# Kernel optimization log

Hardware: AMD Instinct MI355X
Metric: run time of the kernel (lower is better)

## Reference

```python
import jax, jax.numpy as jnp
import numpy as np

NUM_EXPERTS = 8
TOP_K = 2


def setup_inputs() -> dict:
    key = jax.random.key(0)
    k1, k2, k3, k4, k5 = jax.random.split(key, 5)
    B, S, H, F, E = 4, 2048, 1024, 4096, NUM_EXPERTS
    return {
        "hidden_states": jax.random.normal(k1, (B, S, H), dtype=jnp.float32),
        "gate_w": jax.random.normal(k2, (E, H), dtype=jnp.float32) * 0.02,
        "w1": jax.random.normal(k3, (E, F, H), dtype=jnp.float32) * 0.02,
        "w3": jax.random.normal(k4, (E, F, H), dtype=jnp.float32) * 0.02,
        "w2": jax.random.normal(k5, (E, H, F), dtype=jnp.float32) * 0.02,
    }


def reference(hidden_states, gate_w, w1, w3, w2):
    B, S, H = hidden_states.shape
    E = gate_w.shape[0]
    x = hidden_states.reshape(-1, H)  # [T, H]
    T = x.shape[0]

    # Router: logits -> fp32 softmax -> top-k -> renormalize (Mixtral)
    router_logits = x @ gate_w.T  # [T, E]
    probs = jax.nn.softmax(router_logits.astype(jnp.float32), axis=-1)
    top_w, top_idx = jax.lax.top_k(probs, TOP_K)  # [T, K]
    top_w = top_w / jnp.sum(top_w, axis=-1, keepdims=True)
    top_w = top_w.astype(x.dtype)

    # Combine weights per (token, expert); zero for unselected experts.
    comb = jnp.zeros((T, E), dtype=x.dtype).at[
        jnp.arange(T)[:, None], top_idx
    ].add(top_w)  # [T, E]

    out = jnp.zeros((T, H), dtype=x.dtype)
    for e in range(E):  # structural loop over distinct expert weights
        h = jax.nn.silu(x @ w1[e].T) * (x @ w3[e].T)  # [T, F]
        out = out + comb[:, e:e + 1] * (h @ w2[e].T)  # [T, H]

    return out.reshape(B, S, H), router_logits
```

## Files before the change

### kernel.cpp

```cpp
#include <hip/hip_runtime.h>
#include <hip/hip_bf16.h>
#include <stdint.h>

#define T_TOK 8192
#define H_DIM 1024
#define F_DIM 4096
#define NEXP  8
#define CAP        17408
#define CT128      136

typedef __attribute__((ext_vector_type(8))) short bf16x8;
typedef __attribute__((ext_vector_type(4))) float f32x4;

#define AS1 __attribute__((address_space(1)))
#define AS3 __attribute__((address_space(3)))

__device__ __forceinline__ void gload_lds16(const void* g, void* l) {
  __builtin_amdgcn_global_load_lds((const AS1 void*)g, (AS3 void*)l, 16, 0, 0);
}

__device__ __forceinline__ int tile_expert_of(const int* counts, int tm) {
  int row = tm * 128, off = 0, e = NEXP - 1;
#pragma unroll
  for (int k = 0; k < NEXP; ++k) {
    int nxt = off + ((counts[k] + 127) & ~127);
    if (row >= off && row < nxt) { e = k; break; }
    off = nxt;
  }
  return e;
}

struct TK { int i0, i1; float w0, w1; };

__global__ __launch_bounds__(256) void router_kernel(
    const float* __restrict__ x, const float* __restrict__ gw,
    float* __restrict__ logits, int* __restrict__ counts, TK* __restrict__ tk)
{
  const int lane = threadIdx.x & 63;
  const int t = blockIdx.x * 4 + (threadIdx.x >> 6);
  const float* xp = x + (size_t)t * H_DIM;
  float xr[16];
#pragma unroll
  for (int i = 0; i < 16; ++i) xr[i] = xp[lane + i * 64];
  float lg[NEXP];
#pragma unroll
  for (int e = 0; e < NEXP; ++e) {
    const float* gp = gw + e * H_DIM;
    float acc = 0.f;
#pragma unroll
    for (int i = 0; i < 16; ++i) acc += xr[i] * gp[lane + i * 64];
#pragma unroll
    for (int s = 32; s > 0; s >>= 1) acc += __shfl_xor(acc, s, 64);
    lg[e] = acc;
  }
  if (lane < NEXP) logits[(size_t)t * NEXP + lane] = lg[lane];
  if (lane == 0) {
    int i0 = 0; float m0 = lg[0];
#pragma unroll
    for (int e = 1; e < NEXP; ++e) if (lg[e] > m0) { m0 = lg[e]; i0 = e; }
    int i1 = -1; float m1 = -1e30f;
#pragma unroll
    for (int e = 0; e < NEXP; ++e) if (e != i0 && lg[e] > m1) { m1 = lg[e]; i1 = e; }
    float r = expf(m1 - m0);
    float w0 = 1.f / (1.f + r);
    float w1 = r / (1.f + r);
    TK v; v.i0 = i0; v.i1 = i1; v.w0 = w0; v.w1 = w1;
    tk[t] = v;
    atomicAdd(&counts[i0], 1);
    atomicAdd(&counts[i1], 1);
  }
}

__global__ __launch_bounds__(256) void scatter_kernel(
    const TK* __restrict__ tk, const int* __restrict__ counts,
    int* __restrict__ cursor, int* __restrict__ pair_tok,
    float* __restrict__ pair_w, int2* __restrict__ inv)
{
  int t = blockIdx.x * 256 + threadIdx.x;
  if (t >= T_TOK) return;
  int offs[NEXP];
  int o = 0;
#pragma unroll
  for (int e = 0; e < NEXP; ++e) { offs[e] = o; o += (counts[e] + 127) & ~127; }
  TK v = tk[t];
  int p0 = offs[v.i0] + atomicAdd(&cursor[v.i0], 1);
  pair_tok[p0] = t; pair_w[p0] = v.w0;
  int p1 = offs[v.i1] + atomicAdd(&cursor[v.i1], 1);
  pair_tok[p1] = t; pair_w[p1] = v.w1;
  inv[t] = make_int2(p0, p1);
}

union Pack8 { __hip_bfloat16 o[8]; uint4 u; };

__global__ __launch_bounds__(256) void gather_kernel(
    const float* __restrict__ x, const int* __restrict__ pair_tok,
    __hip_bfloat16* __restrict__ xg)
{
  int idx = blockIdx.x * 256 + threadIdx.x;
  int row = idx >> 7;
  int c8  = (idx & 127) << 3;
  int tok = pair_tok[row];
  const float4* src = reinterpret_cast<const float4*>(x + (size_t)tok * H_DIM + c8);
  float4 a = src[0], b = src[1];
  Pack8 pk;
  pk.o[0] = __float2bfloat16(a.x); pk.o[1] = __float2bfloat16(a.y);
  pk.o[2] = __float2bfloat16(a.z); pk.o[3] = __float2bfloat16(a.w);
  pk.o[4] = __float2bfloat16(b.x); pk.o[5] = __float2bfloat16(b.y);
  pk.o[6] = __float2bfloat16(b.z); pk.o[7] = __float2bfloat16(b.w);
  *reinterpret_cast<uint4*>(xg + (size_t)row * H_DIM + c8) = pk.u;
}

__global__ __launch_bounds__(256) void convert3_kernel(
    const float* __restrict__ w1, const float* __restrict__ w3,
    const float* __restrict__ w2, __hip_bfloat16* __restrict__ w1b,
    __hip_bfloat16* __restrict__ w3b, __hip_bfloat16* __restrict__ w2b)
{
  const long long nthr = 3ll * (1 << 22);
  for (long long idx = (long long)blockIdx.x * 256 + threadIdx.x; idx < nthr;
       idx += (long long)gridDim.x * 256) {
    int seg = (int)(idx >> 22);
    long long off = (idx & ((1 << 22) - 1)) * 8;
    const float* src = (seg == 0) ? w1 : (seg == 1) ? w3 : w2;
    __hip_bfloat16* dst = (seg == 0) ? w1b : (seg == 1) ? w3b : w2b;
    float4 a = *reinterpret_cast<const float4*>(src + off);
    float4 b = *reinterpret_cast<const float4*>(src + off + 4);
    Pack8 pk;
    pk.o[0] = __float2bfloat16(a.x); pk.o[1] = __float2bfloat16(a.y);
    pk.o[2] = __float2bfloat16(a.z); pk.o[3] = __float2bfloat16(a.w);
    pk.o[4] = __float2bfloat16(b.x); pk.o[5] = __float2bfloat16(b.y);
    pk.o[6] = __float2bfloat16(b.z); pk.o[7] = __float2bfloat16(b.w);
    *reinterpret_cast<uint4*>(dst + off) = pk.u;
  }
}


__global__ __launch_bounds__(256, 4) void gemm1_kernel(
    const __hip_bfloat16* __restrict__ xg,
    const __hip_bfloat16* __restrict__ w1b,
    const __hip_bfloat16* __restrict__ w3b,
    const int* __restrict__ counts,
    __hip_bfloat16* __restrict__ h)
{
  __shared__ __hip_bfloat16 smem[16384];
  __hip_bfloat16* sA  = smem;
  __hip_bfloat16* sB1 = smem + 8192;
  __hip_bfloat16* sB3 = smem + 12288;

  const int n_  = blockIdx.x;
  const int tm  = n_ >> 6;
  const int tf  = n_ & 63;
  const int e   = tile_expert_of(counts, tm);
  const int tid = threadIdx.x;

  const __hip_bfloat16* A  = xg  + (size_t)tm * 128 * H_DIM;
  const __hip_bfloat16* B1 = w1b + (size_t)e * F_DIM * H_DIM + (size_t)tf * 64 * H_DIM;
  const __hip_bfloat16* B3 = w3b + (size_t)e * F_DIM * H_DIM + (size_t)tf * 64 * H_DIM;

  const int rs  = tid >> 3;
  const int sl  = tid & 7;
  const int xsl = (sl ^ (rs & 7)) * 8;
  const int dst = rs * 64 + sl * 8;

  const int wv = tid >> 6, lane = tid & 63;
  const int wm = wv >> 1, wn = wv & 1;
  const int l16 = lane & 15, lk = lane >> 4;
  const int ps0 = ((0 + lk) ^ (l16 & 7)) * 8;
  const int ps1 = ((4 + lk) ^ (l16 & 7)) * 8;

  f32x4 acc1[4][2] = {};
  f32x4 acc3[4][2] = {};

  for (int kt = 0; kt < H_DIM / 64; ++kt) {
    __syncthreads();
    const int gk = kt * 64 + xsl;
#pragma unroll
    for (int c = 0; c < 4; ++c)
      gload_lds16(A + (size_t)(rs + 32 * c) * H_DIM + gk, &sA[c * 2048 + dst]);
#pragma unroll
    for (int c = 0; c < 2; ++c) {
      gload_lds16(B1 + (size_t)(rs + 32 * c) * H_DIM + gk, &sB1[c * 2048 + dst]);
      gload_lds16(B3 + (size_t)(rs + 32 * c) * H_DIM + gk, &sB3[c * 2048 + dst]);
    }
    __syncthreads();
#pragma unroll
    for (int ks = 0; ks < 2; ++ks) {
      const int ps = ks ? ps1 : ps0;
      bf16x8 a[4], b1[2], b3[2];
#pragma unroll
      for (int m = 0; m < 4; ++m)
        a[m] = *reinterpret_cast<const bf16x8*>(&sA[(wm * 64 + m * 16 + l16) * 64 + ps]);
#pragma unroll
      for (int nf = 0; nf < 2; ++nf) {
        b1[nf] = *reinterpret_cast<const bf16x8*>(&sB1[(wn * 32 + nf * 16 + l16) * 64 + ps]);
        b3[nf] = *reinterpret_cast<const bf16x8*>(&sB3[(wn * 32 + nf * 16 + l16) * 64 + ps]);
      }
#pragma unroll
      for (int m = 0; m < 4; ++m)
#pragma unroll
        for (int nf = 0; nf < 2; ++nf) {
          acc1[m][nf] = __builtin_amdgcn_mfma_f32_16x16x32_bf16(a[m], b1[nf], acc1[m][nf], 0, 0, 0);
          acc3[m][nf] = __builtin_amdgcn_mfma_f32_16x16x32_bf16(a[m], b3[nf], acc3[m][nf], 0, 0, 0);
        }
    }
  }

  __syncthreads();
#pragma unroll
  for (int m = 0; m < 4; ++m)
#pragma unroll
    for (int nf = 0; nf < 2; ++nf)
#pragma unroll
      for (int j = 0; j < 4; ++j) {
        int row = wm * 64 + m * 16 + lk * 4 + j;
        int col = wn * 32 + nf * 16 + l16;
        int phys = row * 64 + (((col >> 3) ^ (row & 7)) << 3) + (col & 7);
        float c1 = acc1[m][nf][j];
        float c3 = acc3[m][nf][j];
        float s  = c1 / (1.f + expf(-c1));
        smem[phys] = __float2bfloat16(s * c3);
      }
  __syncthreads();
  const uint4* s4 = reinterpret_cast<const uint4*>(smem);
  __hip_bfloat16* hp = h + (size_t)tm * 128 * F_DIM + (size_t)tf * 64;
#pragma unroll
  for (int i = 0; i < 4; ++i) {
    int c = i * 256 + tid;
    int row = c >> 3, sg = c & 7;
    *reinterpret_cast<uint4*>(hp + (size_t)row * F_DIM + sg * 8) =
        s4[row * 8 + (sg ^ (row & 7))];
  }
}

__global__ __launch_bounds__(256, 4) void gemm2_kernel(
    const __hip_bfloat16* __restrict__ h,
    const __hip_bfloat16* __restrict__ w2b,
    const int* __restrict__ counts,
    const float* __restrict__ pair_w,
    __hip_bfloat16* __restrict__ y)
{
  __shared__ __hip_bfloat16 smem[16384];
  __hip_bfloat16* sA = smem;
  __hip_bfloat16* sB = smem + 8192;

  const int n_  = blockIdx.x;
  const int r   = n_ & 7;
  const int q   = n_ >> 3;
  const int tm  = (q >> 4) * 8 + r;
  const int s_  = q & 15;
  const int tn  = s_ >> 1;
  const int kh  = s_ & 1;
  const int e   = tile_expert_of(counts, tm);
  const int tid = threadIdx.x;

  const __hip_bfloat16* A = h   + (size_t)tm * 128 * F_DIM + (size_t)kh * 2048;
  const __hip_bfloat16* B = w2b + (size_t)e * H_DIM * F_DIM + (size_t)tn * 128 * F_DIM
                                + (size_t)kh * 2048;

  const int rs  = tid >> 3;
  const int sl  = tid & 7;
  const int xsl = (sl ^ (rs & 7)) * 8;
  const int dst = rs * 64 + sl * 8;

  const int wv = tid >> 6, lane = tid & 63;
  const int wm = wv >> 1, wn = wv & 1;
  const int l16 = lane & 15, lk = lane >> 4;
  const int ps0 = ((0 + lk) ^ (l16 & 7)) * 8;
  const int ps1 = ((4 + lk) ^ (l16 & 7)) * 8;

  f32x4 acc[4][4] = {};

  for (int kt = 0; kt < 2048 / 64; ++kt) {
    __syncthreads();
    const int gk = kt * 64 + xsl;
#pragma unroll
    for (int c = 0; c < 4; ++c) {
      gload_lds16(A + (size_t)(rs + 32 * c) * F_DIM + gk, &sA[c * 2048 + dst]);
      gload_lds16(B + (size_t)(rs + 32 * c) * F_DIM + gk, &sB[c * 2048 + dst]);
    }
    __syncthreads();
#pragma unroll
    for (int ks = 0; ks < 2; ++ks) {
      const int ps = ks ? ps1 : ps0;
      bf16x8 a[4], b[4];
#pragma unroll
      for (int m = 0; m < 4; ++m)
        a[m] = *reinterpret_cast<const bf16x8*>(&sA[(wm * 64 + m * 16 + l16) * 64 + ps]);
#pragma unroll
      for (int nf = 0; nf < 4; ++nf)
        b[nf] = *reinterpret_cast<const bf16x8*>(&sB[(wn * 64 + nf * 16 + l16) * 64 + ps]);
#pragma unroll
      for (int m = 0; m < 4; ++m)
#pragma unroll
        for (int nf = 0; nf < 4; ++nf)
          acc[m][nf] = __builtin_amdgcn_mfma_f32_16x16x32_bf16(a[m], b[nf], acc[m][nf], 0, 0, 0);
    }
  }

  __syncthreads();
#pragma unroll
  for (int m = 0; m < 4; ++m)
#pragma unroll
    for (int j = 0; j < 4; ++j) {
      int row  = wm * 64 + m * 16 + lk * 4 + j;
      float w  = pair_w[tm * 128 + row];
#pragma unroll
      for (int nf = 0; nf < 4; ++nf) {
        int col  = wn * 64 + nf * 16 + l16;
        int phys = row * 128 + (((col >> 3) ^ (row & 7)) << 3) + (col & 7);
        smem[phys] = __float2bfloat16(w * acc[m][nf][j]);
      }
    }
  __syncthreads();
  const uint4* s4 = reinterpret_cast<const uint4*>(smem);
  __hip_bfloat16* yp = y + (size_t)kh * CAP * H_DIM
                         + (size_t)tm * 128 * H_DIM + (size_t)tn * 128;
#pragma unroll
  for (int i = 0; i < 8; ++i) {
    int c = i * 256 + tid;
    int row = c >> 4, sg = c & 15;
    *reinterpret_cast<uint4*>(yp + (size_t)row * H_DIM + sg * 8) =
        s4[row * 16 + ((sg & 8) | ((sg ^ row) & 7))];
  }
}

__global__ __launch_bounds__(256) void combine_kernel(
    const __hip_bfloat16* __restrict__ y, const int2* __restrict__ inv,
    float* __restrict__ out)
{
  int idx = blockIdx.x * 256 + threadIdx.x;
  int t  = idx >> 7;
  int c8 = (idx & 127) << 3;
  int2 p = inv[t];
  const __hip_bfloat16* y1 = y + (size_t)CAP * H_DIM;
  union { uint4 u; __hip_bfloat16 o[8]; } a, b, c, d;
  a.u = *reinterpret_cast<const uint4*>(y  + (size_t)p.x * H_DIM + c8);
  b.u = *reinterpret_cast<const uint4*>(y  + (size_t)p.y * H_DIM + c8);
  c.u = *reinterpret_cast<const uint4*>(y1 + (size_t)p.x * H_DIM + c8);
  d.u = *reinterpret_cast<const uint4*>(y1 + (size_t)p.y * H_DIM + c8);
  float* op = out + (size_t)t * H_DIM + c8;
#pragma unroll
  for (int i = 0; i < 8; ++i)
    op[i] = __bfloat162float(a.o[i]) + __bfloat162float(b.o[i]) +
            __bfloat162float(c.o[i]) + __bfloat162float(d.o[i]);
}

#define WS_COUNTS   0
#define WS_CURSOR   32
#define WS_TK       1024
#define WS_PAIRTOK  132096
#define WS_PAIRW    201728
#define WS_ZERO_BYTES 271360
#define WS_INV      271360
#define WS_XG       336896ll
#define WS_W1       (WS_XG + 35651584ll)
#define WS_W3       (WS_W1 + 67108864ll)
#define WS_W2       (WS_W3 + 67108864ll)
#define WS_H        (WS_W2 + 67108864ll)
#define WS_Y        WS_XG

extern "C" void kernel_launch(void* const* d_in, const int* in_sizes, int n_in,
                              void* d_out, int out_size, void* d_ws, size_t ws_size,
                              hipStream_t stream) {
  const float* x  = (const float*)d_in[0];
  const float* gw = (const float*)d_in[1];
  const float* w1 = (const float*)d_in[2];
  const float* w3 = (const float*)d_in[3];
  const float* w2 = (const float*)d_in[4];
  float* out    = (float*)d_out;
  float* logits = out + (size_t)T_TOK * H_DIM;

  char* ws = (char*)d_ws;
  int*   counts   = (int*)(ws + WS_COUNTS);
  int*   cursor   = (int*)(ws + WS_CURSOR);
  TK*    tk       = (TK*)(ws + WS_TK);
  int*   pair_tok = (int*)(ws + WS_PAIRTOK);
  float* pair_w   = (float*)(ws + WS_PAIRW);
  int2*  inv      = (int2*)(ws + WS_INV);
  __hip_bfloat16* xg  = (__hip_bfloat16*)(ws + WS_XG);
  __hip_bfloat16* w1b = (__hip_bfloat16*)(ws + WS_W1);
  __hip_bfloat16* w3b = (__hip_bfloat16*)(ws + WS_W3);
  __hip_bfloat16* w2b = (__hip_bfloat16*)(ws + WS_W2);
  __hip_bfloat16* hbuf = (__hip_bfloat16*)(ws + WS_H);
  __hip_bfloat16* ybuf = (__hip_bfloat16*)(ws + WS_Y);

  hipMemsetAsync(d_ws, 0, WS_ZERO_BYTES, stream);

  router_kernel<<<T_TOK / 4, 256, 0, stream>>>(x, gw, logits, counts, tk);
  scatter_kernel<<<T_TOK / 256, 256, 0, stream>>>(tk, counts, cursor,
                                                  pair_tok, pair_w, inv);
  gather_kernel<<<(CAP * 128) / 256, 256, 0, stream>>>(x, pair_tok, xg);

  convert3_kernel<<<8192, 256, 0, stream>>>(w1, w3, w2, w1b, w3b, w2b);

  gemm1_kernel<<<CT128 * (F_DIM / 64), 256, 0, stream>>>(
      xg, w1b, w3b, counts, hbuf);
  gemm2_kernel<<<CT128 * 16, 256, 0, stream>>>(
      hbuf, w2b, counts, pair_w, ybuf);
  combine_kernel<<<(T_TOK * H_DIM / 8) / 256, 256, 0, stream>>>(ybuf, inv, out);
}
```

Before: 866.4 us.

## Enlarge gemm1 tiles to 256x128 with double-buffered LDS pipeline

Pads expert segments to 256 rows and rewrites the gate/up GEMM to use 512-thread blocks computing 256x128 tiles. The K loop now double-buffers LDS and interleaves the global-to-LDS loads for the next step with the MFMA work of the current step, using split barriers and s_setprio. This aims to raise data reuse per block and hide load latency. In exchange it adds more padding rows, raises register and LDS pressure, and leaves fewer blocks in the grid.

```diff
diff --git a/kernel.cpp b/kernel.cpp
--- a/kernel.cpp
+++ b/kernel.cpp
@@ -6,8 +6,9 @@
 #define H_DIM 1024
 #define F_DIM 4096
 #define NEXP  8
-#define CAP        17408
-#define CT128      136
+#define CAP        18432
+#define CT256      72
+#define CT128      144
 
 typedef __attribute__((ext_vector_type(8))) short bf16x8;
 typedef __attribute__((ext_vector_type(4))) float f32x4;
@@ -19,11 +20,11 @@
   __builtin_amdgcn_global_load_lds((const AS1 void*)g, (AS3 void*)l, 16, 0, 0);
 }
 
-__device__ __forceinline__ int tile_expert_of(const int* counts, int tm) {
-  int row = tm * 128, off = 0, e = NEXP - 1;
+__device__ __forceinline__ int expert_of_row(const int* counts, int row) {
+  int off = 0, e = NEXP - 1;
 #pragma unroll
   for (int k = 0; k < NEXP; ++k) {
-    int nxt = off + ((counts[k] + 127) & ~127);
+    int nxt = off + ((counts[k] + 255) & ~255);
     if (row >= off && row < nxt) { e = k; break; }
     off = nxt;
   }
@@ -81,7 +82,7 @@
   int offs[NEXP];
   int o = 0;
 #pragma unroll
-  for (int e = 0; e < NEXP; ++e) { offs[e] = o; o += (counts[e] + 127) & ~127; }
+  for (int e = 0; e < NEXP; ++e) { offs[e] = o; o += (counts[e] + 255) & ~255; }
   TK v = tk[t];
   int p0 = offs[v.i0] + atomicAdd(&cursor[v.i0], 1);
   pair_tok[p0] = t; pair_w[p0] = v.w0;
@@ -134,27 +135,25 @@
 }
 
 
-__global__ __launch_bounds__(256, 4) void gemm1_kernel(
+__global__ __launch_bounds__(512, 2) void gemm1_kernel(
     const __hip_bfloat16* __restrict__ xg,
     const __hip_bfloat16* __restrict__ w1b,
     const __hip_bfloat16* __restrict__ w3b,
     const int* __restrict__ counts,
     __hip_bfloat16* __restrict__ h)
 {
-  __shared__ __hip_bfloat16 smem[16384];
-  __hip_bfloat16* sA  = smem;
-  __hip_bfloat16* sB1 = smem + 8192;
-  __hip_bfloat16* sB3 = smem + 12288;
-
-  const int n_  = blockIdx.x;
-  const int tm  = n_ >> 6;
-  const int tf  = n_ & 63;
-  const int e   = tile_expert_of(counts, tm);
+  __shared__ __hip_bfloat16 sA[2][256 * 64];
+  __shared__ __hip_bfloat16 sB[2][256 * 64];
+
+  const int n_ = blockIdx.x;
+  const int tm = n_ >> 5;
+  const int tf = n_ & 31;
+  const int e  = expert_of_row(counts, tm * 256);
   const int tid = threadIdx.x;
 
-  const __hip_bfloat16* A  = xg  + (size_t)tm * 128 * H_DIM;
-  const __hip_bfloat16* B1 = w1b + (size_t)e * F_DIM * H_DIM + (size_t)tf * 64 * H_DIM;
-  const __hip_bfloat16* B3 = w3b + (size_t)e * F_DIM * H_DIM + (size_t)tf * 64 * H_DIM;
+  const __hip_bfloat16* A  = xg  + (size_t)tm * 256 * H_DIM;
+  const __hip_bfloat16* B1 = w1b + (size_t)e * F_DIM * H_DIM + (size_t)tf * 128 * H_DIM;
+  const __hip_bfloat16* B3 = w3b + (size_t)e * F_DIM * H_DIM + (size_t)tf * 128 * H_DIM;
 
   const int rs  = tid >> 3;
   const int sl  = tid & 7;
@@ -162,73 +161,102 @@
   const int dst = rs * 64 + sl * 8;
 
   const int wv = tid >> 6, lane = tid & 63;
-  const int wm = wv >> 1, wn = wv & 1;
+  const int wm = wv >> 2, wn = wv & 3;
   const int l16 = lane & 15, lk = lane >> 4;
   const int ps0 = ((0 + lk) ^ (l16 & 7)) * 8;
   const int ps1 = ((4 + lk) ^ (l16 & 7)) * 8;
 
-  f32x4 acc1[4][2] = {};
-  f32x4 acc3[4][2] = {};
-
-  for (int kt = 0; kt < H_DIM / 64; ++kt) {
-    __syncthreads();
-    const int gk = kt * 64 + xsl;
-#pragma unroll
-    for (int c = 0; c < 4; ++c)
-      gload_lds16(A + (size_t)(rs + 32 * c) * H_DIM + gk, &sA[c * 2048 + dst]);
-#pragma unroll
-    for (int c = 0; c < 2; ++c) {
-      gload_lds16(B1 + (size_t)(rs + 32 * c) * H_DIM + gk, &sB1[c * 2048 + dst]);
-      gload_lds16(B3 + (size_t)(rs + 32 * c) * H_DIM + gk, &sB3[c * 2048 + dst]);
-    }
-    __syncthreads();
-#pragma unroll
-    for (int ks = 0; ks < 2; ++ks) {
-      const int ps = ks ? ps1 : ps0;
-      bf16x8 a[4], b1[2], b3[2];
-#pragma unroll
-      for (int m = 0; m < 4; ++m)
-        a[m] = *reinterpret_cast<const bf16x8*>(&sA[(wm * 64 + m * 16 + l16) * 64 + ps]);
-#pragma unroll
-      for (int nf = 0; nf < 2; ++nf) {
-        b1[nf] = *reinterpret_cast<const bf16x8*>(&sB1[(wn * 32 + nf * 16 + l16) * 64 + ps]);
-        b3[nf] = *reinterpret_cast<const bf16x8*>(&sB3[(wn * 32 + nf * 16 + l16) * 64 + ps]);
+  f32x4 acc1[8][2] = {};
+  f32x4 acc3[8][2] = {};
+  bf16x8 a[4][2], b[2][2];
+
+#define ST_A01(bb, gg) { \
+    gload_lds16(A + (size_t)rs * H_DIM + (gg) + xsl,          &sA[bb][dst]); \
+    gload_lds16(A + (size_t)(64 + rs) * H_DIM + (gg) + xsl,   &sA[bb][4096 + dst]); }
+#define ST_A23(bb, gg) { \
+    gload_lds16(A + (size_t)(128 + rs) * H_DIM + (gg) + xsl,  &sA[bb][8192 + dst]); \
+    gload_lds16(A + (size_t)(192 + rs) * H_DIM + (gg) + xsl,  &sA[bb][12288 + dst]); }
+#define ST_B1(bb, gg) { \
+    gload_lds16(B1 + (size_t)rs * H_DIM + (gg) + xsl,         &sB[bb][dst]); \
+    gload_lds16(B1 + (size_t)(64 + rs) * H_DIM + (gg) + xsl,  &sB[bb][4096 + dst]); }
+#define ST_B3(bb, gg) { \
+    gload_lds16(B3 + (size_t)rs * H_DIM + (gg) + xsl,         &sB[bb][8192 + dst]); \
+    gload_lds16(B3 + (size_t)(64 + rs) * H_DIM + (gg) + xsl,  &sB[bb][12288 + dst]); }
+#define RD_A(cur, mh) { \
+    _Pragma("unroll") for (int f2 = 0; f2 < 4; ++f2) { \
+      int ro = (wm * 128 + (mh) * 64 + f2 * 16 + l16) * 64; \
+      a[f2][0] = *reinterpret_cast<const bf16x8*>(&sA[cur][ro + ps0]); \
+      a[f2][1] = *reinterpret_cast<const bf16x8*>(&sA[cur][ro + ps1]); } }
+#define RD_B(cur, half) { \
+    _Pragma("unroll") for (int nf = 0; nf < 2; ++nf) { \
+      int ro = ((half) * 128 + wn * 32 + nf * 16 + l16) * 64; \
+      b[nf][0] = *reinterpret_cast<const bf16x8*>(&sB[cur][ro + ps0]); \
+      b[nf][1] = *reinterpret_cast<const bf16x8*>(&sB[cur][ro + ps1]); } }
+#define MMA(ACC, mh) { __builtin_amdgcn_s_setprio(1); \
+    _Pragma("unroll") for (int f2 = 0; f2 < 4; ++f2) \
+    _Pragma("unroll") for (int nf = 0; nf < 2; ++nf) { \
+      ACC[(mh) * 4 + f2][nf] = __builtin_amdgcn_mfma_f32_16x16x32_bf16(a[f2][0], b[nf][0], ACC[(mh) * 4 + f2][nf], 0, 0, 0); \
+      ACC[(mh) * 4 + f2][nf] = __builtin_amdgcn_mfma_f32_16x16x32_bf16(a[f2][1], b[nf][1], ACC[(mh) * 4 + f2][nf], 0, 0, 0); } \
+    __builtin_amdgcn_s_setprio(0); }
+
+  ST_A01(0, 0); ST_A23(0, 0); ST_B1(0, 0); ST_B3(0, 0);
+  asm volatile("s_waitcnt vmcnt(0)" ::: "memory");
+  __builtin_amdgcn_s_barrier();
+
+  for (int t = 0; t < 16; ++t) {
+    const int cur = t & 1, nb = cur ^ 1;
+    const int gg = (t < 15 ? t + 1 : 15) * 64;
+    ST_A01(nb, gg);
+    asm volatile("s_waitcnt vmcnt(2)" ::: "memory");
+    RD_A(cur, 0); RD_B(cur, 0); MMA(acc1, 0);
+    __builtin_amdgcn_s_barrier();
+    ST_A23(nb, gg);
+    RD_A(cur, 1); MMA(acc1, 1);
+    __builtin_amdgcn_s_barrier();
+    ST_B1(nb, gg);
+    RD_B(cur, 1); MMA(acc3, 1);
+    __builtin_amdgcn_s_barrier();
+    ST_B3(nb, gg);
+    RD_A(cur, 0); MMA(acc3, 0);
+    __builtin_amdgcn_s_barrier();
+  }
+
+  asm volatile("s_waitcnt vmcnt(0)" ::: "memory");
+  __builtin_amdgcn_s_barrier();
+
+  __hip_bfloat16* bounce = &sA[0][0];
+#pragma unroll
+  for (int f = 0; f < 8; ++f)
+#pragma unroll
+    for (int nf = 0; nf < 2; ++nf)
+#pragma unroll
+      for (int j = 0; j < 4; ++j) {
+        int row = wm * 128 + f * 16 + lk * 4 + j;
+        int col = wn * 32 + nf * 16 + l16;
+        int slot = col >> 3;
+        int phys = row * 128 + (((slot & 8) | ((slot ^ row) & 7)) << 3) + (col & 7);
+        float c1 = acc1[f][nf][j];
+        float c3 = acc3[f][nf][j];
+        float s  = c1 / (1.f + expf(-c1));
+        bounce[phys] = __float2bfloat16(s * c3);
       }
-#pragma unroll
-      for (int m = 0; m < 4; ++m)
-#pragma unroll
-        for (int nf = 0; nf < 2; ++nf) {
-          acc1[m][nf] = __builtin_amdgcn_mfma_f32_16x16x32_bf16(a[m], b1[nf], acc1[m][nf], 0, 0, 0);
-          acc3[m][nf] = __builtin_amdgcn_mfma_f32_16x16x32_bf16(a[m], b3[nf], acc3[m][nf], 0, 0, 0);
-        }
-    }
-  }
-
-  __syncthreads();
-#pragma unroll
-  for (int m = 0; m < 4; ++m)
-#pragma unroll
-    for (int nf = 0; nf < 2; ++nf)
-#pragma unroll
-      for (int j = 0; j < 4; ++j) {
-        int row = wm * 64 + m * 16 + lk * 4 + j;
-        int col = wn * 32 + nf * 16 + l16;
-        int phys = row * 64 + (((col >> 3) ^ (row & 7)) << 3) + (col & 7);
-        float c1 = acc1[m][nf][j];
-        float c3 = acc3[m][nf][j];
-        float s  = c1 / (1.f + expf(-c1));
-        smem[phys] = __float2bfloat16(s * c3);
-      }
-  __syncthreads();
-  const uint4* s4 = reinterpret_cast<const uint4*>(smem);
-  __hip_bfloat16* hp = h + (size_t)tm * 128 * F_DIM + (size_t)tf * 64;
-#pragma unroll
-  for (int i = 0; i < 4; ++i) {
-    int c = i * 256 + tid;
-    int row = c >> 3, sg = c & 7;
+  __builtin_amdgcn_s_barrier();
+  const uint4* s4 = reinterpret_cast<const uint4*>(bounce);
+  __hip_bfloat16* hp = h + (size_t)tm * 256 * F_DIM + (size_t)tf * 128;
+#pragma unroll
+  for (int i = 0; i < 8; ++i) {
+    int c = i * 512 + tid;
+    int row = c >> 4, sg = c & 15;
     *reinterpret_cast<uint4*>(hp + (size_t)row * F_DIM + sg * 8) =
-        s4[row * 8 + (sg ^ (row & 7))];
-  }
+        s4[row * 16 + ((sg & 8) | ((sg ^ row) & 7))];
+  }
+#undef ST_A01
+#undef ST_A23
+#undef ST_B1
+#undef ST_B3
+#undef RD_A
+#undef RD_B
+#undef MMA
 }
 
 __global__ __launch_bounds__(256, 4) void gemm2_kernel(
@@ -249,7 +277,7 @@
   const int s_  = q & 15;
   const int tn  = s_ >> 1;
   const int kh  = s_ & 1;
-  const int e   = tile_expert_of(counts, tm);
+  const int e   = expert_of_row(counts, tm * 128);
   const int tid = threadIdx.x;
 
   const __hip_bfloat16* A = h   + (size_t)tm * 128 * F_DIM + (size_t)kh * 2048;
@@ -348,11 +376,11 @@
 #define WS_CURSOR   32
 #define WS_TK       1024
 #define WS_PAIRTOK  132096
-#define WS_PAIRW    201728
-#define WS_ZERO_BYTES 271360
-#define WS_INV      271360
-#define WS_XG       336896ll
-#define WS_W1       (WS_XG + 35651584ll)
+#define WS_PAIRW    205824
+#define WS_ZERO_BYTES 279552
+#define WS_INV      279552
+#define WS_XG       345088ll
+#define WS_W1       (WS_XG + 37748736ll)
 #define WS_W3       (WS_W1 + 67108864ll)
 #define WS_W2       (WS_W3 + 67108864ll)
 #define WS_H        (WS_W2 + 67108864ll)
@@ -392,7 +420,7 @@
 
   convert3_kernel<<<8192, 256, 0, stream>>>(w1, w3, w2, w1b, w3b, w2b);
 
-  gemm1_kernel<<<CT128 * (F_DIM / 64), 256, 0, stream>>>(
+  gemm1_kernel<<<CT256 * (F_DIM / 128), 512, 0, stream>>>(
       xg, w1b, w3b, counts, hbuf);
   gemm2_kernel<<<CT128 * 16, 256, 0, stream>>>(
       hbuf, w2b, counts, pair_w, ybuf);
```

Result: slower. 1.052 ms (+21.4%).
